# Kernel tuning notes

Measured on AMD Instinct MI355X. Metric: run time of the kernel, lower is better.

The kernel has to match this reference:

```python
import jax, jax.numpy as jnp
import numpy as np

EPS = 1e-7  # K.epsilon()
B, S, W1, W2, D = 256, 4, 64, 128, 300
HID = 4


def setup_inputs() -> dict:
    key = jax.random.key(0)
    k1, k2, k3, k4, k5, k6, k7 = jax.random.split(key, 7)
    return {
        "tuple1": jax.random.normal(k1, (B, S, W1, D), dtype=jnp.float32),
        "tuple2": jax.random.normal(k2, (B, S, W2, D), dtype=jnp.float32),
        "mask1": jax.random.randint(k3, (B, S, W1), 0, 2, dtype=jnp.int32),
        "mask2": jax.random.randint(k4, (B, S, W2), 0, 2, dtype=jnp.int32),
        "threshold": jax.random.normal(k5, (), dtype=jnp.float32),
        "W_hidden": jax.random.normal(k6, (S, HID), dtype=jnp.float32) * 0.5,
        "W_score": jax.random.normal(k7, (HID, 1), dtype=jnp.float32) * 0.5,
    }


def reference(tuple1, tuple2, mask1, mask2, threshold, W_hidden, W_score):
    # Pairwise dot-product similarity between every tuple1 word and tuple2 word per slot.
    sim = jnp.einsum("bswd,bsvd->bswv", tuple1, tuple2)  # (B, S, W1, W2)
    m1 = mask1.astype(jnp.float32)
    m2 = mask2.astype(jnp.float32)
    overlap = (sim >= threshold).astype(jnp.float32)
    overlap = overlap * m1[:, :, :, None] * m2[:, :, None, :]
    slot_overlap = jnp.sum(overlap, axis=(2, 3))  # (B, S)
    count1 = jnp.sum(m1, axis=2)  # (B, S)
    divisor = jnp.where(count1 == 0, EPS, count1)
    normalized = slot_overlap / divisor  # (B, S)
    h = jnp.tanh(normalized @ W_hidden)  # (B, HID)
    return jax.nn.sigmoid(h @ W_score)  # (B, 1)
```

## Files before the change

### kernel.cpp

```cpp
#include <hip/hip_runtime.h>
#include <math.h>

#define B_   256
#define S_   4
#define W1_  64
#define W2_  128
#define D_   300
#define HID_ 4

typedef float          fx4   __attribute__((ext_vector_type(4)));
typedef short          s16x8 __attribute__((ext_vector_type(8)));
typedef unsigned int   ux4   __attribute__((ext_vector_type(4)));

__device__ __forceinline__ unsigned bf16_rne(float x) {
    unsigned u = __float_as_uint(x);
    return (u + 0x7FFFu + ((u >> 16) & 1u)) >> 16;
}

__device__ __forceinline__ void cvt8(const fx4 x0, const fx4 x1, s16x8& hi, s16x8& lo) {
    ux4 hu, lu;
#pragma unroll
    for (int p = 0; p < 4; ++p) {
        float a = (p < 2) ? x0[2 * p]     : x1[2 * p - 4];
        float b = (p < 2) ? x0[2 * p + 1] : x1[2 * p - 3];
        unsigned ha = bf16_rne(a), hb = bf16_rne(b);
        float haf = __uint_as_float(ha << 16);
        float hbf = __uint_as_float(hb << 16);
        unsigned la = bf16_rne(a - haf), lb = bf16_rne(b - hbf);
        hu[p] = ha | (hb << 16);
        lu[p] = la | (lb << 16);
    }
    hi = __builtin_bit_cast(s16x8, hu);
    lo = __builtin_bit_cast(s16x8, lu);
}

__global__ __launch_bounds__(256, 2) void sim_count_mfma(
    const float* __restrict__ t1, const float* __restrict__ t2,
    const int* __restrict__ m1, const int* __restrict__ m2,
    const float* __restrict__ thr_p, int* __restrict__ cnt)
{
    const int slot = blockIdx.x;
    const int tid  = threadIdx.x;
    const int l    = tid & 63;
    const int w    = tid >> 6;
    const int rowHalf = w >> 1, colHalf = w & 1;
    const int lr   = l & 15;
    const int lg8  = (l >> 4) * 8;
    const float thr = *thr_p;

    const float* aP[2];
    const float* bP[4];
#pragma unroll
    for (int rt = 0; rt < 2; ++rt)
        aP[rt] = t1 + (size_t)slot * W1_ * D_ + (size_t)(rowHalf * 32 + rt * 16 + lr) * D_ + lg8;
#pragma unroll
    for (int ct = 0; ct < 4; ++ct)
        bP[ct] = t2 + (size_t)slot * W2_ * D_ + (size_t)(colHalf * 64 + ct * 16 + lr) * D_ + lg8;

    fx4 acc[2][4];
#pragma unroll
    for (int rt = 0; rt < 2; ++rt)
#pragma unroll
        for (int ct = 0; ct < 4; ++ct) {
            fx4 z; z[0] = 0.f; z[1] = 0.f; z[2] = 0.f; z[3] = 0.f;
            acc[rt][ct] = z;
        }

    auto issue_full = [&](fx4 (&SA)[2][2], fx4 (&SB)[4][2], int t) {
#pragma unroll
        for (int rt = 0; rt < 2; ++rt) {
            const float* p = aP[rt] + t * 32;
            SA[rt][0] = *(const fx4*)p;
            SA[rt][1] = *(const fx4*)(p + 4);
        }
#pragma unroll
        for (int ct = 0; ct < 4; ++ct) {
            const float* p = bP[ct] + t * 32;
            SB[ct][0] = *(const fx4*)p;
            SB[ct][1] = *(const fx4*)(p + 4);
        }
    };
    auto issue_tail = [&](fx4 (&SA)[2][2], fx4 (&SB)[4][2]) {
        fx4 z; z[0] = 0.f; z[1] = 0.f; z[2] = 0.f; z[3] = 0.f;
#pragma unroll
        for (int rt = 0; rt < 2; ++rt) {
            const float* p = aP[rt] + 288;
            SA[rt][0] = z; SA[rt][1] = z;
            if (lg8 < 16) SA[rt][0] = *(const fx4*)p;
            if (lg8 == 0) SA[rt][1] = *(const fx4*)(p + 4);
        }
#pragma unroll
        for (int ct = 0; ct < 4; ++ct) {
            const float* p = bP[ct] + 288;
            SB[ct][0] = z; SB[ct][1] = z;
            if (lg8 < 16) SB[ct][0] = *(const fx4*)p;
            if (lg8 == 0) SB[ct][1] = *(const fx4*)(p + 4);
        }
    };
    auto compute = [&](fx4 (&SA)[2][2], fx4 (&SB)[4][2]) {
        s16x8 ah[2], al[2];
#pragma unroll
        for (int rt = 0; rt < 2; ++rt) cvt8(SA[rt][0], SA[rt][1], ah[rt], al[rt]);
#pragma unroll
        for (int ct = 0; ct < 4; ++ct) {
            s16x8 bh, bl;
            cvt8(SB[ct][0], SB[ct][1], bh, bl);
#pragma unroll
            for (int rt = 0; rt < 2; ++rt) {
                acc[rt][ct] = __builtin_amdgcn_mfma_f32_16x16x32_bf16(ah[rt], bh, acc[rt][ct], 0, 0, 0);
                acc[rt][ct] = __builtin_amdgcn_mfma_f32_16x16x32_bf16(ah[rt], bl, acc[rt][ct], 0, 0, 0);
                acc[rt][ct] = __builtin_amdgcn_mfma_f32_16x16x32_bf16(al[rt], bh, acc[rt][ct], 0, 0, 0);
            }
        }
    };

    fx4 s0A[2][2], s0B[4][2], s1A[2][2], s1B[4][2];
    issue_full(s0A, s0B, 0);
#pragma unroll
    for (int tt = 0; tt < 4; ++tt) {
        issue_full(s1A, s1B, 2 * tt + 1);
        compute(s0A, s0B);
        issue_full(s0A, s0B, 2 * tt + 2);
        compute(s1A, s1B);
    }
    issue_tail(s1A, s1B);
    compute(s0A, s0B);
    compute(s1A, s1B);

    int am[2][4];
#pragma unroll
    for (int rt = 0; rt < 2; ++rt)
#pragma unroll
        for (int r = 0; r < 4; ++r)
            am[rt][r] = m1[slot * W1_ + rowHalf * 32 + rt * 16 + (l >> 4) * 4 + r];
    int bm[4];
#pragma unroll
    for (int ct = 0; ct < 4; ++ct)
        bm[ct] = m2[slot * W2_ + colHalf * 64 + ct * 16 + lr];

    int lc = 0;
#pragma unroll
    for (int rt = 0; rt < 2; ++rt)
#pragma unroll
        for (int ct = 0; ct < 4; ++ct)
#pragma unroll
            for (int r = 0; r < 4; ++r)
                lc += ((acc[rt][ct][r] >= thr) & (am[rt][r] != 0) & (bm[ct] != 0)) ? 1 : 0;
#pragma unroll
    for (int o = 32; o > 0; o >>= 1) lc += __shfl_down(lc, o);
    if (l == 0) atomicAdd(&cnt[slot], lc);
}

__global__ __launch_bounds__(256) void finalize_head(
    const int* __restrict__ cnt, const int* __restrict__ m1,
    const float* __restrict__ Wh,
    const float* __restrict__ Ws,
    float* __restrict__ out)
{
    int b = blockIdx.x * blockDim.x + threadIdx.x;
    if (b >= B_) return;
    float n[4];
#pragma unroll
    for (int s = 0; s < 4; ++s) {
        const int slot = b * 4 + s;
        int nA = 0;
        const int4* mp = (const int4*)(m1 + slot * W1_);
#pragma unroll
        for (int g = 0; g < 16; ++g) {
            int4 v = mp[g];
            nA += (v.x != 0) + (v.y != 0) + (v.z != 0) + (v.w != 0);
        }
        const float divisor = (nA == 0) ? 1e-7f : (float)nA;
        n[s] = (float)cnt[slot] / divisor;
    }
    float score = 0.f;
#pragma unroll
    for (int j = 0; j < HID_; ++j) {
        float h = n[0] * Wh[0 * HID_ + j] + n[1] * Wh[1 * HID_ + j]
                + n[2] * Wh[2 * HID_ + j] + n[3] * Wh[3 * HID_ + j];
        h = tanhf(h);
        score += h * Ws[j];
    }
    out[b] = 1.f / (1.f + expf(-score));
}

extern "C" void kernel_launch(void* const* d_in, const int* in_sizes, int n_in,
                              void* d_out, int out_size, void* d_ws, size_t ws_size,
                              hipStream_t stream)
{
    const float* t1  = (const float*)d_in[0];
    const float* t2  = (const float*)d_in[1];
    const int*   m1  = (const int*)d_in[2];
    const int*   m2  = (const int*)d_in[3];
    const float* thr = (const float*)d_in[4];
    const float* Wh  = (const float*)d_in[5];
    const float* Ws  = (const float*)d_in[6];
    float* out = (float*)d_out;
    int*   cnt = (int*)d_ws;

    hipMemsetAsync(cnt, 0, B_ * S_ * sizeof(int), stream);
    sim_count_mfma<<<B_ * S_, 256, 0, stream>>>(t1, t2, m1, m2, thr, cnt);
    finalize_head<<<1, 256, 0, stream>>>(cnt, m1, Wh, Ws, out);
}
```

Before: 340.8 us.

## Triple-buffer global loads with inline asm and explicit vmcnt waits

Replaces the compiler-scheduled double-buffered register prefetch with a three-stage pipeline. Each stage's loads are issued as inline-asm global_load_dwordx4 with immediate offsets, and sched_barrier plus explicit s_waitcnt vmcnt fences stop the compiler from collapsing the overlap. This keeps roughly two K-chunks of loads in flight during each MFMA compute step to hide memory latency. The extra buffer raises register pressure under launch_bounds(256,2), and the tail chunk is still loaded without overlap.

```diff
diff --git a/kernel.cpp b/kernel.cpp
--- a/kernel.cpp
+++ b/kernel.cpp
@@ -33,6 +33,26 @@
     hi = __builtin_bit_cast(s16x8, hu);
     lo = __builtin_bit_cast(s16x8, lu);
 }
+
+template <int OFF>
+__device__ __forceinline__ void gload(fx4& d, const float* p) {
+    asm volatile("global_load_dwordx4 %0, %1, off offset:%c2"
+                 : "=v"(d) : "v"(p), "i"(OFF));
+}
+
+#define FENCE  __builtin_amdgcn_sched_barrier(0)
+#define WAIT24 do { asm volatile("s_waitcnt vmcnt(24)" ::: "memory"); FENCE; } while (0)
+#define WAIT12 do { asm volatile("s_waitcnt vmcnt(12)" ::: "memory"); FENCE; } while (0)
+#define WAIT0  do { asm volatile("s_waitcnt vmcnt(0)"  ::: "memory"); FENCE; } while (0)
+
+#define ISSUE(T, AA, BB) do { \
+    gload<(T)*128>(AA[0][0], aP0); gload<(T)*128+16>(AA[0][1], aP0); \
+    gload<(T)*128>(AA[1][0], aP1); gload<(T)*128+16>(AA[1][1], aP1); \
+    gload<(T)*128>(BB[0][0], bP0); gload<(T)*128+16>(BB[0][1], bP0); \
+    gload<(T)*128>(BB[1][0], bP1); gload<(T)*128+16>(BB[1][1], bP1); \
+    gload<(T)*128>(BB[2][0], bP2); gload<(T)*128+16>(BB[2][1], bP2); \
+    gload<(T)*128>(BB[3][0], bP3); gload<(T)*128+16>(BB[3][1], bP3); \
+    FENCE; } while (0)
 
 __global__ __launch_bounds__(256, 2) void sim_count_mfma(
     const float* __restrict__ t1, const float* __restrict__ t2,
@@ -46,16 +66,15 @@
     const int rowHalf = w >> 1, colHalf = w & 1;
     const int lr   = l & 15;
     const int lg8  = (l >> 4) * 8;
-    const float thr = *thr_p;
-
-    const float* aP[2];
-    const float* bP[4];
-#pragma unroll
-    for (int rt = 0; rt < 2; ++rt)
-        aP[rt] = t1 + (size_t)slot * W1_ * D_ + (size_t)(rowHalf * 32 + rt * 16 + lr) * D_ + lg8;
-#pragma unroll
-    for (int ct = 0; ct < 4; ++ct)
-        bP[ct] = t2 + (size_t)slot * W2_ * D_ + (size_t)(colHalf * 64 + ct * 16 + lr) * D_ + lg8;
+
+    const float* t1b = t1 + (size_t)slot * W1_ * D_;
+    const float* t2b = t2 + (size_t)slot * W2_ * D_;
+    const float* aP0 = t1b + (size_t)(rowHalf * 32 +  0 + lr) * D_ + lg8;
+    const float* aP1 = t1b + (size_t)(rowHalf * 32 + 16 + lr) * D_ + lg8;
+    const float* bP0 = t2b + (size_t)(colHalf * 64 +  0 + lr) * D_ + lg8;
+    const float* bP1 = t2b + (size_t)(colHalf * 64 + 16 + lr) * D_ + lg8;
+    const float* bP2 = t2b + (size_t)(colHalf * 64 + 32 + lr) * D_ + lg8;
+    const float* bP3 = t2b + (size_t)(colHalf * 64 + 48 + lr) * D_ + lg8;
 
     fx4 acc[2][4];
 #pragma unroll
@@ -66,37 +85,6 @@
             acc[rt][ct] = z;
         }
 
-    auto issue_full = [&](fx4 (&SA)[2][2], fx4 (&SB)[4][2], int t) {
-#pragma unroll
-        for (int rt = 0; rt < 2; ++rt) {
-            const float* p = aP[rt] + t * 32;
-            SA[rt][0] = *(const fx4*)p;
-            SA[rt][1] = *(const fx4*)(p + 4);
-        }
-#pragma unroll
-        for (int ct = 0; ct < 4; ++ct) {
-            const float* p = bP[ct] + t * 32;
-            SB[ct][0] = *(const fx4*)p;
-            SB[ct][1] = *(const fx4*)(p + 4);
-        }
-    };
-    auto issue_tail = [&](fx4 (&SA)[2][2], fx4 (&SB)[4][2]) {
-        fx4 z; z[0] = 0.f; z[1] = 0.f; z[2] = 0.f; z[3] = 0.f;
-#pragma unroll
-        for (int rt = 0; rt < 2; ++rt) {
-            const float* p = aP[rt] + 288;
-            SA[rt][0] = z; SA[rt][1] = z;
-            if (lg8 < 16) SA[rt][0] = *(const fx4*)p;
-            if (lg8 == 0) SA[rt][1] = *(const fx4*)(p + 4);
-        }
-#pragma unroll
-        for (int ct = 0; ct < 4; ++ct) {
-            const float* p = bP[ct] + 288;
-            SB[ct][0] = z; SB[ct][1] = z;
-            if (lg8 < 16) SB[ct][0] = *(const fx4*)p;
-            if (lg8 == 0) SB[ct][1] = *(const fx4*)(p + 4);
-        }
-    };
     auto compute = [&](fx4 (&SA)[2][2], fx4 (&SB)[4][2]) {
         s16x8 ah[2], al[2];
 #pragma unroll
@@ -114,19 +102,46 @@
         }
     };
 
-    fx4 s0A[2][2], s0B[4][2], s1A[2][2], s1B[4][2];
-    issue_full(s0A, s0B, 0);
-#pragma unroll
-    for (int tt = 0; tt < 4; ++tt) {
-        issue_full(s1A, s1B, 2 * tt + 1);
-        compute(s0A, s0B);
-        issue_full(s0A, s0B, 2 * tt + 2);
-        compute(s1A, s1B);
-    }
-    issue_tail(s1A, s1B);
-    compute(s0A, s0B);
-    compute(s1A, s1B);
-
+    fx4 A0[2][2], B0[4][2], A1[2][2], B1[4][2], A2[2][2], B2[4][2];
+
+    ISSUE(0, A0, B0);
+    ISSUE(1, A1, B1);
+    ISSUE(2, A2, B2);
+    WAIT24; compute(A0, B0); FENCE; ISSUE(3, A0, B0);
+    WAIT24; compute(A1, B1); FENCE; ISSUE(4, A1, B1);
+    WAIT24; compute(A2, B2); FENCE; ISSUE(5, A2, B2);
+    WAIT24; compute(A0, B0); FENCE; ISSUE(6, A0, B0);
+    WAIT24; compute(A1, B1); FENCE; ISSUE(7, A1, B1);
+    WAIT24; compute(A2, B2); FENCE; ISSUE(8, A2, B2);
+    WAIT24; compute(A0, B0); FENCE;
+    WAIT12; compute(A1, B1); FENCE;
+    WAIT0;  compute(A2, B2); FENCE;
+
+    {
+        fx4 z; z[0] = 0.f; z[1] = 0.f; z[2] = 0.f; z[3] = 0.f;
+        A0[0][0] = z; A0[0][1] = z; A0[1][0] = z; A0[1][1] = z;
+        B0[0][0] = z; B0[0][1] = z; B0[1][0] = z; B0[1][1] = z;
+        B0[2][0] = z; B0[2][1] = z; B0[3][0] = z; B0[3][1] = z;
+        if (lg8 < 16) {
+            A0[0][0] = *(const fx4*)(aP0 + 288);
+            A0[1][0] = *(const fx4*)(aP1 + 288);
+            B0[0][0] = *(const fx4*)(bP0 + 288);
+            B0[1][0] = *(const fx4*)(bP1 + 288);
+            B0[2][0] = *(const fx4*)(bP2 + 288);
+            B0[3][0] = *(const fx4*)(bP3 + 288);
+        }
+        if (lg8 == 0) {
+            A0[0][1] = *(const fx4*)(aP0 + 292);
+            A0[1][1] = *(const fx4*)(aP1 + 292);
+            B0[0][1] = *(const fx4*)(bP0 + 292);
+            B0[1][1] = *(const fx4*)(bP1 + 292);
+            B0[2][1] = *(const fx4*)(bP2 + 292);
+            B0[3][1] = *(const fx4*)(bP3 + 292);
+        }
+        compute(A0, B0);
+    }
+
+    const float thr = *thr_p;
     int am[2][4];
 #pragma unroll
     for (int rt = 0; rt < 2; ++rt)
```

Result: faster. 306.9 us (-9.9%).
